# Optimization experiments

Hardware: AMD Instinct MI355X
Metric: run time of the kernel (lower is better)

The kernel has to match this reference:

```python
import jax, jax.numpy as jnp
import numpy as np
import math

D_MODEL = 2048
N_HEADS = 32
N_KV_HEADS = 8
HEAD_DIM = D_MODEL // N_HEADS  # 64
GROUPS = N_HEADS // N_KV_HEADS  # 4
WINDOW = 512


def setup_inputs() -> dict:
    key = jax.random.key(0)
    k0, k1, k2, k3, k4 = jax.random.split(key, 5)
    B, T = 1, 2048
    scale = 0.02
    return {
        "hidden_states": jax.random.normal(k0, (B, T, D_MODEL), dtype=jnp.float32),
        "Wq": jax.random.normal(k1, (D_MODEL, D_MODEL), dtype=jnp.float32) * scale,
        "Wk": jax.random.normal(k2, (N_KV_HEADS * HEAD_DIM, D_MODEL), dtype=jnp.float32) * scale,
        "Wv": jax.random.normal(k3, (N_KV_HEADS * HEAD_DIM, D_MODEL), dtype=jnp.float32) * scale,
        "Wo": jax.random.normal(k4, (D_MODEL, D_MODEL), dtype=jnp.float32) * scale,
    }


def _rope_tables(T, dim):
    # matches RotaryEmbedding: inv_freq over even indices, emb = cat(freqs, freqs)
    inv_freq = 1.0 / (10000.0 ** (jnp.arange(0, dim, 2, dtype=jnp.float32) / dim))
    freqs = jnp.arange(T, dtype=jnp.float32)[:, None] * inv_freq[None, :]  # [T, dim/2]
    emb = jnp.concatenate([freqs, freqs], axis=-1)  # [T, dim]
    return jnp.cos(emb), jnp.sin(emb)


def _rotate_half(x):
    d = x.shape[-1] // 2
    return jnp.concatenate([-x[..., d:], x[..., :d]], axis=-1)


def reference(hidden_states, Wq, Wk, Wv, Wo):
    B, T, _ = hidden_states.shape
    # projections (torch Linear: y = x @ W^T)
    q = (hidden_states @ Wq.T).reshape(B, T, N_HEADS, HEAD_DIM).transpose(0, 2, 1, 3)      # [B,H,T,D]
    k = (hidden_states @ Wk.T).reshape(B, T, N_KV_HEADS, HEAD_DIM).transpose(0, 2, 1, 3)   # [B,Hkv,T,D]
    v = (hidden_states @ Wv.T).reshape(B, T, N_KV_HEADS, HEAD_DIM).transpose(0, 2, 1, 3)
    # RoPE (cos/sin broadcast [T,D] over [B,H,T,D])
    cos, sin = _rope_tables(T, HEAD_DIM)
    q = q * cos + _rotate_half(q) * sin
    k = k * cos + _rotate_half(k) * sin
    # GQA: expand KV heads
    k = jnp.repeat(k, GROUPS, axis=1)  # [B,H,T,D]
    v = jnp.repeat(v, GROUPS, axis=1)
    scores = jnp.einsum('bhqd,bhkd->bhqk', q, k) / math.sqrt(HEAD_DIM)  # [B,H,T,T]
    if WINDOW < T:
        i = jnp.arange(T)[:, None]
        j = jnp.arange(T)[None, :]
        # row i keeps columns [max(0,i-W/2), min(T,i+W/2)) — same as the torch loop
        allowed = (j >= i - WINDOW // 2) & (j < i + WINDOW // 2)
        scores = jnp.where(allowed, scores, -jnp.inf)
    w = jax.nn.softmax(scores, axis=-1)
    out = jnp.einsum('bhqk,bhkd->bhqd', w, v)  # [B,H,T,D]
    out = out.transpose(0, 2, 1, 3).reshape(B, T, D_MODEL)
    return out @ Wo.T
```

## Files before the change

### kernel.cpp

```cpp
#include <hip/hip_runtime.h>
#include <math.h>

#define TLEN 2048
#define DMODEL 2048
#define NHEADS 32
#define NKV 8
#define HDIM 64
#define KVDIM 512
#define WHALF 256

typedef short shortx8 __attribute__((ext_vector_type(8)));
typedef float floatx4 __attribute__((ext_vector_type(4)));
typedef unsigned int uint32;

__device__ __forceinline__ unsigned short f2bf_rne(float x) {
    union { float f; uint32 u; } v; v.f = x;
    uint32 r = v.u + 0x7FFFu + ((v.u >> 16) & 1u);
    return (unsigned short)(r >> 16);
}

#define GL16(g, l)                                                              \
    __builtin_amdgcn_global_load_lds(                                           \
        (const __attribute__((address_space(1))) unsigned int*)(g),             \
        (__attribute__((address_space(3))) unsigned int*)(l), 16, 0, 0)

__global__ __launch_bounds__(256) void convert_inputs(const float* __restrict__ hs,
                                                      const float* __restrict__ Wq,
                                                      const float* __restrict__ Wk,
                                                      const float* __restrict__ Wv,
                                                      const float* __restrict__ Wo,
                                                      unsigned short* __restrict__ hsb,
                                                      unsigned short* __restrict__ Wcat,
                                                      unsigned short* __restrict__ Wob) {
    int b = blockIdx.x;
    const float* src; unsigned short* dst;
    if (b < 512)       { src = hs; dst = hsb; }
    else if (b < 1024) { src = Wq; dst = Wcat;                           b -= 512; }
    else if (b < 1152) { src = Wk; dst = Wcat + (size_t)2048 * DMODEL;   b -= 1024; }
    else if (b < 1280) { src = Wv; dst = Wcat + (size_t)2560 * DMODEL;   b -= 1152; }
    else               { src = Wo; dst = Wob;                            b -= 1280; }
    size_t base = (size_t)b * 8192 + threadIdx.x * 4;
#pragma unroll
    for (int it = 0; it < 8; ++it) {
        size_t off = base + (size_t)it * 1024;
        float4 v = *(const float4*)(src + off);
        short4 p;
        p.x = (short)f2bf_rne(v.x); p.y = (short)f2bf_rne(v.y);
        p.z = (short)f2bf_rne(v.z); p.w = (short)f2bf_rne(v.w);
        *(short4*)(dst + off) = p;
    }
}

__global__ __launch_bounds__(256) void gemm_qkv(const unsigned short* __restrict__ hsb,
                                                const unsigned short* __restrict__ Wcat,
                                                unsigned short* __restrict__ Qo,
                                                unsigned short* __restrict__ Ko,
                                                unsigned short* __restrict__ Vo) {
    __shared__ short Ah[128][128];
    __shared__ short Bh[64][128];

    const int bnx = blockIdx.x;
    int mode, coff;
    if (bnx < 32)      { mode = 0; coff = bnx * 64; }
    else if (bnx < 40) { mode = 1; coff = (bnx - 32) * 64; }
    else               { mode = 2; coff = (bnx - 40) * 64; }
    const unsigned short* Bbase = Wcat + (size_t)bnx * 64 * DMODEL;

    const int bm = blockIdx.y * 128;
    const int tid = threadIdx.x;
    const int w = tid >> 6, lane = tid & 63;
    const int wA = w * 32, wB = w * 16;
    const int lr = lane & 15, quad = lane >> 4;
    const int r4 = lane >> 4;

    const unsigned short* Ag[4];
    const unsigned short* Bg[4];
#pragma unroll
    for (int gm = 0; gm < 4; ++gm) {
        const int cof = ((lane & 15) ^ r4 ^ (gm << 2)) * 8;
        Ag[gm] = hsb   + (size_t)(bm + wA + 4 * gm + r4) * DMODEL + cof;
        Bg[gm] = Bbase + (size_t)(wB + 4 * gm + r4) * DMODEL + cof;
    }

    floatx4 acc[2][4];
#pragma unroll
    for (int i = 0; i < 2; ++i)
#pragma unroll
        for (int j = 0; j < 4; ++j) acc[i][j] = (floatx4)0.0f;

    for (int k0 = 0; k0 < DMODEL; k0 += 128) {
        __syncthreads();
#pragma unroll
        for (int q = 0; q < 2; ++q)
#pragma unroll
            for (int gm = 0; gm < 4; ++gm)
                GL16(Ag[gm] + (size_t)(16 * q) * DMODEL + k0, &Ah[wA + 16 * q + 4 * gm][0]);
#pragma unroll
        for (int gm = 0; gm < 4; ++gm)
            GL16(Bg[gm] + k0, &Bh[wB + 4 * gm][0]);
        __syncthreads();

#pragma unroll
        for (int s = 0; s < 4; ++s) {
            const int cs = ((s * 4 + quad) ^ lr) * 8;
            shortx8 a0 = *(shortx8*)&Ah[wA + lr][cs];
            shortx8 a1 = *(shortx8*)&Ah[wA + 16 + lr][cs];
            shortx8 bf[4];
#pragma unroll
            for (int j = 0; j < 4; ++j) bf[j] = *(shortx8*)&Bh[j * 16 + lr][cs];
#pragma unroll
            for (int j = 0; j < 4; ++j)
                acc[0][j] = __builtin_amdgcn_mfma_f32_16x16x32_bf16(a0, bf[j], acc[0][j], 0, 0, 0);
#pragma unroll
            for (int j = 0; j < 4; ++j)
                acc[1][j] = __builtin_amdgcn_mfma_f32_16x16x32_bf16(a1, bf[j], acc[1][j], 0, 0, 0);
        }
    }

    if (mode != 2) {
#pragma unroll
        for (int j = 0; j < 2; ++j) {
            float fr = exp2f(-(float)(j * 16 + lr) * (13.2877123795494f / 32.0f));
#pragma unroll
            for (int i = 0; i < 2; ++i) {
                const int row0 = bm + wA + i * 16 + quad * 4;
#pragma unroll
                for (int r = 0; r < 4; ++r) {
                    float s, c;
                    sincosf((float)(row0 + r) * fr, &s, &c);
                    float x1 = acc[i][j][r], x2 = acc[i][j + 2][r];
                    acc[i][j][r]     = x1 * c - x2 * s;
                    acc[i][j + 2][r] = x2 * c + x1 * s;
                }
            }
        }
    }

#pragma unroll
    for (int i = 0; i < 2; ++i) {
        const int row0 = bm + wA + i * 16 + quad * 4;
        if (mode == 0) {
#pragma unroll
            for (int j = 0; j < 4; ++j) {
                int col = coff + j * 16 + lr;
#pragma unroll
                for (int r = 0; r < 4; ++r)
                    Qo[(size_t)(row0 + r) * DMODEL + col] = f2bf_rne(0.125f * acc[i][j][r]);
            }
        } else if (mode == 1) {
#pragma unroll
            for (int j = 0; j < 4; ++j) {
                int col = coff + j * 16 + lr;
#pragma unroll
                for (int r = 0; r < 4; ++r)
                    Ko[(size_t)(row0 + r) * KVDIM + col] = f2bf_rne(acc[i][j][r]);
            }
        } else {
#pragma unroll
            for (int j = 0; j < 4; ++j) {
                int col = coff + j * 16 + lr;
                short4 pk;
                pk.x = (short)f2bf_rne(acc[i][j][0]);
                pk.y = (short)f2bf_rne(acc[i][j][1]);
                pk.z = (short)f2bf_rne(acc[i][j][2]);
                pk.w = (short)f2bf_rne(acc[i][j][3]);
                *(short4*)&Vo[(size_t)col * TLEN + row0] = pk;
            }
        }
    }
}

__global__ __launch_bounds__(512) void attn_mfma(const unsigned short* __restrict__ Qb,
                                                 const unsigned short* __restrict__ Kb,
                                                 const unsigned short* __restrict__ Vt,
                                                 unsigned short* __restrict__ Ab) {
    __shared__ short Qs[128][64];
    __shared__ short Ks[64][64];
    __shared__ short Vs[64][64];
    __shared__ short Ps[128][72];

    const int h = blockIdx.y, q0 = blockIdx.x * 128, kvh = h >> 2;
    const int tid = threadIdx.x;
    const int w = tid >> 6, lane = tid & 63;
    const int l15 = lane & 15, quad = lane >> 4;
    const int qw = q0 + w * 16;

    const int sr  = lane >> 3;
    const int sgc = ((lane & 7) ^ sr) * 8;

    {
        const unsigned short* qsrc = Qb + (size_t)(qw + sr) * DMODEL + h * HDIM + sgc;
        GL16(qsrc,              &Qs[w * 16 + 0][0]);
        GL16(qsrc + 8 * DMODEL, &Qs[w * 16 + 8][0]);
    }

    floatx4 o[4];
#pragma unroll
    for (int j = 0; j < 4; ++j) o[j] = (floatx4)0.0f;
    float l_lane[4] = {0.0f, 0.0f, 0.0f, 0.0f};

    for (int c = 0; c < 10; ++c) {
        const int ch0 = q0 - WHALF + c * 64;
        if (ch0 < 0 || ch0 >= TLEN) continue;

        __syncthreads();
        {
            const unsigned short* ksrc = Kb + (size_t)(ch0 + w * 8 + sr) * KVDIM + kvh * HDIM + sgc;
            const unsigned short* vsrc = Vt + (size_t)(kvh * HDIM + w * 8 + sr) * TLEN + ch0 + sgc;
            GL16(ksrc, &Ks[w * 8][0]);
            GL16(vsrc, &Vs[w * 8][0]);
        }
        __syncthreads();

        if (ch0 >= qw - 319 && ch0 <= qw + 270) {
            floatx4 sacc[4];
#pragma unroll
            for (int t = 0; t < 4; ++t) sacc[t] = (floatx4)0.0f;
#pragma unroll
            for (int s = 0; s < 2; ++s) {
                const int cs = ((s * 4 + quad) ^ (l15 & 7)) * 8;
                shortx8 aq = *(shortx8*)&Qs[w * 16 + l15][cs];
#pragma unroll
                for (int t = 0; t < 4; ++t) {
                    shortx8 bk = *(shortx8*)&Ks[t * 16 + l15][cs];
                    sacc[t] = __builtin_amdgcn_mfma_f32_16x16x32_bf16(aq, bk, sacc[t], 0, 0, 0);
                }
            }

#pragma unroll
            for (int r = 0; r < 4; ++r) {
                const int q = qw + quad * 4 + r;
#pragma unroll
                for (int t = 0; t < 4; ++t) {
                    const int k = ch0 + t * 16 + l15;
                    bool valid = (k >= q - WHALF) && (k < q + WHALF);
                    float p = valid ? __expf(sacc[t][r]) : 0.0f;
                    l_lane[r] += p;
                    Ps[w * 16 + quad * 4 + r][t * 16 + l15] = (short)f2bf_rne(p);
                }
            }

#pragma unroll
            for (int ks = 0; ks < 2; ++ks) {
                const int cs = ((ks * 4 + quad) ^ (l15 & 7)) * 8;
                shortx8 ap = *(shortx8*)&Ps[w * 16 + l15][ks * 32 + quad * 8];
#pragma unroll
                for (int j = 0; j < 4; ++j) {
                    shortx8 bv = *(shortx8*)&Vs[j * 16 + l15][cs];
                    o[j] = __builtin_amdgcn_mfma_f32_16x16x32_bf16(ap, bv, o[j], 0, 0, 0);
                }
            }
        }
    }

#pragma unroll
    for (int r = 0; r < 4; ++r) {
        float l = l_lane[r];
#pragma unroll
        for (int mb = 1; mb < 16; mb <<= 1)
            l += __shfl_xor(l, mb, 64);
        float inv = 1.0f / l;
        const int q = qw + quad * 4 + r;
#pragma unroll
        for (int j = 0; j < 4; ++j)
            Ab[(size_t)q * DMODEL + h * HDIM + j * 16 + l15] = f2bf_rne(o[j][r] * inv);
    }
}

__global__ __launch_bounds__(256) void gemm_oproj(const unsigned short* __restrict__ Ab,
                                                  const unsigned short* __restrict__ Wob,
                                                  float* __restrict__ C) {
    __shared__ short Ah[128][128];
    __shared__ short Bh[64][128];

    const int bm = blockIdx.y * 128, bn = blockIdx.x * 64;
    const int tid = threadIdx.x;
    const int w = tid >> 6, lane = tid & 63;
    const int wA = w * 32, wB = w * 16;
    const int lr = lane & 15, quad = lane >> 4;
    const int r4 = lane >> 4;

    const unsigned short* Ag[4];
    const unsigned short* Bg[4];
#pragma unroll
    for (int gm = 0; gm < 4; ++gm) {
        const int cof = ((lane & 15) ^ r4 ^ (gm << 2)) * 8;
        Ag[gm] = Ab  + (size_t)(bm + wA + 4 * gm + r4) * DMODEL + cof;
        Bg[gm] = Wob + (size_t)(bn + wB + 4 * gm + r4) * DMODEL + cof;
    }

    floatx4 acc[2][4];
#pragma unroll
    for (int i = 0; i < 2; ++i)
#pragma unroll
        for (int j = 0; j < 4; ++j) acc[i][j] = (floatx4)0.0f;

    for (int k0 = 0; k0 < DMODEL; k0 += 128) {
        __syncthreads();
#pragma unroll
        for (int q = 0; q < 2; ++q)
#pragma unroll
            for (int gm = 0; gm < 4; ++gm)
                GL16(Ag[gm] + (size_t)(16 * q) * DMODEL + k0, &Ah[wA + 16 * q + 4 * gm][0]);
#pragma unroll
        for (int gm = 0; gm < 4; ++gm)
            GL16(Bg[gm] + k0, &Bh[wB + 4 * gm][0]);
        __syncthreads();

#pragma unroll
        for (int s = 0; s < 4; ++s) {
            const int cs = ((s * 4 + quad) ^ lr) * 8;
            shortx8 a0 = *(shortx8*)&Ah[wA + lr][cs];
            shortx8 a1 = *(shortx8*)&Ah[wA + 16 + lr][cs];
            shortx8 bf[4];
#pragma unroll
            for (int j = 0; j < 4; ++j) bf[j] = *(shortx8*)&Bh[j * 16 + lr][cs];
#pragma unroll
            for (int j = 0; j < 4; ++j)
                acc[0][j] = __builtin_amdgcn_mfma_f32_16x16x32_bf16(a0, bf[j], acc[0][j], 0, 0, 0);
#pragma unroll
            for (int j = 0; j < 4; ++j)
                acc[1][j] = __builtin_amdgcn_mfma_f32_16x16x32_bf16(a1, bf[j], acc[1][j], 0, 0, 0);
        }
    }

#pragma unroll
    for (int i = 0; i < 2; ++i) {
        const int row0 = bm + wA + i * 16 + quad * 4;
#pragma unroll
        for (int j = 0; j < 4; ++j) {
            int col = bn + j * 16 + lr;
#pragma unroll
            for (int r = 0; r < 4; ++r)
                C[(size_t)(row0 + r) * DMODEL + col] = acc[i][j][r];
        }
    }
}

extern "C" void kernel_launch(void* const* d_in, const int* in_sizes, int n_in,
                              void* d_out, int out_size, void* d_ws, size_t ws_size,
                              hipStream_t stream) {
    const float* hs = (const float*)d_in[0];
    const float* Wq = (const float*)d_in[1];
    const float* Wk = (const float*)d_in[2];
    const float* Wv = (const float*)d_in[3];
    const float* Wo = (const float*)d_in[4];
    float* out = (float*)d_out;

    unsigned short* Qb   = (unsigned short*)d_ws;
    unsigned short* Kb   = Qb + (size_t)TLEN * DMODEL;
    unsigned short* Vt   = Kb + (size_t)TLEN * KVDIM;
    unsigned short* hsAb = Vt + (size_t)KVDIM * TLEN;
    unsigned short* Wcat = hsAb + (size_t)TLEN * DMODEL;
    unsigned short* Wob  = Wcat + (size_t)3072 * DMODEL;

    dim3 blk(256);

    convert_inputs<<<1792, blk, 0, stream>>>(hs, Wq, Wk, Wv, Wo, hsAb, Wcat, Wob);

    gemm_qkv<<<dim3(48, TLEN / 128), blk, 0, stream>>>(hsAb, Wcat, Qb, Kb, Vt);

    attn_mfma<<<dim3(TLEN / 128, NHEADS), dim3(512), 0, stream>>>(Qb, Kb, Vt, hsAb);

    gemm_oproj<<<dim3(DMODEL / 64, TLEN / 128), blk, 0, stream>>>(hsAb, Wob, out);
}
```

Before: 183.2 us.

## Double-buffer K/V tiles in attention and swizzle P shared-memory layout

```diff
diff --git a/kernel.cpp b/kernel.cpp
--- a/kernel.cpp
+++ b/kernel.cpp
@@ -175,8 +175,8 @@
                                                  const unsigned short* __restrict__ Vt,
                                                  unsigned short* __restrict__ Ab) {
     __shared__ short Qs[128][64];
-    __shared__ short Ks[64][64];
-    __shared__ short Vs[64][64];
+    __shared__ short Ks[2][64][64];
+    __shared__ short Vs[2][64][64];
     __shared__ short Ps[128][72];
 
     const int h = blockIdx.y, q0 = blockIdx.x * 128, kvh = h >> 2;
@@ -188,10 +188,26 @@
     const int sr  = lane >> 3;
     const int sgc = ((lane & 7) ^ sr) * 8;
 
+    int cb = q0 - WHALF; if (cb < 0) cb = 0;
+    int ce = q0 + 128 + WHALF; if (ce > TLEN) ce = TLEN;
+
+    const unsigned short* kbase = Kb + (size_t)(w * 8 + sr) * KVDIM + kvh * HDIM + sgc;
+    const unsigned short* vbase = Vt + (size_t)(kvh * HDIM + w * 8 + sr) * TLEN + sgc;
+
     {
         const unsigned short* qsrc = Qb + (size_t)(qw + sr) * DMODEL + h * HDIM + sgc;
         GL16(qsrc,              &Qs[w * 16 + 0][0]);
         GL16(qsrc + 8 * DMODEL, &Qs[w * 16 + 8][0]);
+        GL16(kbase + (size_t)cb * KVDIM, &Ks[0][w * 8][0]);
+        GL16(vbase + cb,                 &Vs[0][w * 8][0]);
+    }
+    __syncthreads();
+
+    shortx8 aq[2];
+#pragma unroll
+    for (int s = 0; s < 2; ++s) {
+        const int cs = ((s * 4 + quad) ^ (l15 & 7)) * 8;
+        aq[s] = *(shortx8*)&Qs[w * 16 + l15][cs];
     }
 
     floatx4 o[4];
@@ -199,18 +215,12 @@
     for (int j = 0; j < 4; ++j) o[j] = (floatx4)0.0f;
     float l_lane[4] = {0.0f, 0.0f, 0.0f, 0.0f};
 
-    for (int c = 0; c < 10; ++c) {
-        const int ch0 = q0 - WHALF + c * 64;
-        if (ch0 < 0 || ch0 >= TLEN) continue;
-
-        __syncthreads();
-        {
-            const unsigned short* ksrc = Kb + (size_t)(ch0 + w * 8 + sr) * KVDIM + kvh * HDIM + sgc;
-            const unsigned short* vsrc = Vt + (size_t)(kvh * HDIM + w * 8 + sr) * TLEN + ch0 + sgc;
-            GL16(ksrc, &Ks[w * 8][0]);
-            GL16(vsrc, &Vs[w * 8][0]);
-        }
-        __syncthreads();
+    int p = 0;
+    for (int ch0 = cb; ch0 < ce; ch0 += 64) {
+        if (ch0 + 64 < ce) {
+            GL16(kbase + (size_t)(ch0 + 64) * KVDIM, &Ks[p ^ 1][w * 8][0]);
+            GL16(vbase + (ch0 + 64),                 &Vs[p ^ 1][w * 8][0]);
+        }
 
         if (ch0 >= qw - 319 && ch0 <= qw + 270) {
             floatx4 sacc[4];
@@ -219,38 +229,44 @@
 #pragma unroll
             for (int s = 0; s < 2; ++s) {
                 const int cs = ((s * 4 + quad) ^ (l15 & 7)) * 8;
-                shortx8 aq = *(shortx8*)&Qs[w * 16 + l15][cs];
 #pragma unroll
                 for (int t = 0; t < 4; ++t) {
-                    shortx8 bk = *(shortx8*)&Ks[t * 16 + l15][cs];
-                    sacc[t] = __builtin_amdgcn_mfma_f32_16x16x32_bf16(aq, bk, sacc[t], 0, 0, 0);
+                    shortx8 bk = *(shortx8*)&Ks[p][t * 16 + l15][cs];
+                    sacc[t] = __builtin_amdgcn_mfma_f32_16x16x32_bf16(aq[s], bk, sacc[t], 0, 0, 0);
                 }
             }
 
 #pragma unroll
             for (int r = 0; r < 4; ++r) {
                 const int q = qw + quad * 4 + r;
+                const int prow = w * 16 + quad * 4 + r;
+                const int rsw = (quad * 4 + r) & 7;
 #pragma unroll
                 for (int t = 0; t < 4; ++t) {
                     const int k = ch0 + t * 16 + l15;
                     bool valid = (k >= q - WHALF) && (k < q + WHALF);
-                    float p = valid ? __expf(sacc[t][r]) : 0.0f;
-                    l_lane[r] += p;
-                    Ps[w * 16 + quad * 4 + r][t * 16 + l15] = (short)f2bf_rne(p);
+                    float pv = valid ? __expf(sacc[t][r]) : 0.0f;
+                    l_lane[r] += pv;
+                    const int g = t * 2 + (l15 >> 3);
+                    Ps[prow][((g ^ rsw) * 8) + (l15 & 7)] = (short)f2bf_rne(pv);
                 }
             }
 
 #pragma unroll
             for (int ks = 0; ks < 2; ++ks) {
                 const int cs = ((ks * 4 + quad) ^ (l15 & 7)) * 8;
-                shortx8 ap = *(shortx8*)&Ps[w * 16 + l15][ks * 32 + quad * 8];
+                const int pg = ((ks * 4 + quad) ^ (l15 & 7)) * 8;
+                shortx8 ap = *(shortx8*)&Ps[w * 16 + l15][pg];
 #pragma unroll
                 for (int j = 0; j < 4; ++j) {
-                    shortx8 bv = *(shortx8*)&Vs[j * 16 + l15][cs];
+                    shortx8 bv = *(shortx8*)&Vs[p][j * 16 + l15][cs];
                     o[j] = __builtin_amdgcn_mfma_f32_16x16x32_bf16(ap, bv, o[j], 0, 0, 0);
                 }
             }
         }
+
+        __syncthreads();
+        p ^= 1;
     }
 
 #pragma unroll
```

After: 181.8 us, median of 2. No clear change (-0.8%).
